# Kernel optimization log

Hardware: AMD Instinct MI355X
Metric: run time of the kernel (lower is better)

## Reference

```python
import jax, jax.numpy as jnp
import numpy as np

B, C, H, W = 8, 512, 96, 96
CK, CV, K = 64, 64, 3  # key/value channels = C/8, kernel_size=3


def setup_inputs() -> dict:
    key = jax.random.key(0)
    ks = jax.random.split(key, 11)
    p = lambda k, shape: jax.random.normal(k, shape, dtype=jnp.float32) * 0.05
    return {
        "x": jax.random.normal(ks[0], (B, C, H, W), dtype=jnp.float32),
        "key1_w": p(ks[1], (CK, C, 1, 1)),
        "key1_b": p(ks[2], (CK,)),
        "key_dw_w": p(ks[3], (CK, 1, K, K)),
        "key_dw_b": p(ks[4], (CK,)),
        "key3_w": p(ks[5], (K * K, CK, 1, 1)),
        "key3_b": p(ks[6], (K * K,)),
        "value_w": p(ks[7], (CV, C, 1, 1)),
        "value_b": p(ks[8], (CV,)),
        "out_w": p(ks[9], (C, CV, 1, 1)),
        "out_b": p(ks[10], (C,)),
    }


def _conv1x1(x, w, b):
    # x: [B,Cin,H,W], w: [Cout,Cin,1,1]
    return jnp.einsum('bchw,oc->bohw', x, w[:, :, 0, 0]) + b[None, :, None, None]


def _unfold3(x):
    # nn.Unfold(kernel_size=3, stride=1, padding=1) then view -> [B,C,9,H,W]
    b, c, h, w = x.shape
    xp = jnp.pad(x, ((0, 0), (0, 0), (1, 1), (1, 1)))
    patches = [xp[:, :, i:i + h, j:j + w] for i in range(3) for j in range(3)]
    return jnp.stack(patches, axis=2)  # [B,C,9,H,W], row-major kernel order like torch


def reference(x, key1_w, key1_b, key_dw_w, key_dw_b, key3_w, key3_b,
              value_w, value_b, out_w, out_b):
    # key branch: 1x1 conv + ReLU -> depthwise 3x3 (no act) -> 1x1 -> k^2 logits
    k = jax.nn.relu(_conv1x1(x, key1_w, key1_b))
    k = jax.lax.conv_general_dilated(
        k, key_dw_w, window_strides=(1, 1), padding='SAME',
        feature_group_count=CK,
        dimension_numbers=('NCHW', 'OIHW', 'NCHW')) + key_dw_b[None, :, None, None]
    k = _conv1x1(k, key3_w, key3_b)            # [B,9,H,W]
    weights = jax.nn.softmax(k[:, None], axis=2)  # [B,1,9,H,W], softmax over kernel taps

    # value branch: 1x1 conv (no act) then unfold 3x3 neighborhoods
    v = _unfold3(_conv1x1(x, value_w, value_b))   # [B,CV,9,H,W]

    y = jnp.sum(weights * v, axis=2)              # [B,CV,H,W]
    return x + _conv1x1(y, out_w, out_b)
```

## Files before the change

### kernel.cpp

```cpp
#include <hip/hip_runtime.h>

#define B_ 8
#define C_ 512
#define H_ 96
#define W_ 96
#define HW_ (H_ * W_)
#define CK_ 64

typedef __attribute__((ext_vector_type(8))) short bf16x8;
typedef __attribute__((ext_vector_type(4))) float f32x4;

#define WPK_OFF ((size_t)192 * HW_)

__device__ __forceinline__ short f2bf(float f) {
    union { float f; unsigned u; } v; v.f = f;
    unsigned r = v.u + 0x7fffu + ((v.u >> 16) & 1u);
    return (short)(r >> 16);
}

__device__ __forceinline__ bf16x8 cvt8(float4 a, float4 b) {
    bf16x8 s;
    s[0] = f2bf(a.x); s[1] = f2bf(a.y); s[2] = f2bf(a.z); s[3] = f2bf(a.w);
    s[4] = f2bf(b.x); s[5] = f2bf(b.y); s[6] = f2bf(b.z); s[7] = f2bf(b.w);
    return s;
}


__global__ void pack_w_kernel(const float* __restrict__ key1_w,
                              const float* __restrict__ value_w,
                              float* __restrict__ outbuf)
{
    const int idx = blockIdx.x * 256 + threadIdx.x;
    const int c8  = idx >> 7;
    const int oc  = idx & 127;
    const float* src = (oc < 64) ? (key1_w + (size_t)oc * C_)
                                 : (value_w + (size_t)(oc - 64) * C_);
    float4 f0 = *(const float4*)(src + c8 * 8);
    float4 f1 = *(const float4*)(src + c8 * 8 + 4);
    short* wpk = (short*)(outbuf + WPK_OFF);
    *(bf16x8*)(wpk + (size_t)idx * 8) = cvt8(f0, f1);
}

__global__ __launch_bounds__(256, 4)
void kv_conv_mfma(const float* __restrict__ x,
                  const float* __restrict__ key1_b,
                  const float* __restrict__ value_b,
                  float* __restrict__ outbuf)
{
    const int b    = blockIdx.y;
    const int px0  = blockIdx.x * 64;
    const int tid  = threadIdx.x;
    const int lane = tid & 63;
    const int w    = tid >> 6;
    const int wm   = w & 1;
    const int wn   = w >> 1;
    const int l15  = lane & 15;
    const int q    = lane >> 4;

    __shared__ float s_bias[128];
    if (tid < 128) s_bias[tid] = (tid < 64) ? key1_b[tid] : value_b[tid - 64];
    __syncthreads();

    f32x4 acc[4][2];
#pragma unroll
    for (int i = 0; i < 4; ++i)
#pragma unroll
        for (int j = 0; j < 2; ++j) acc[i][j] = (f32x4){0.f, 0.f, 0.f, 0.f};

    const short* wpk = (const short*)(outbuf + WPK_OFF);
    const short* apk = wpk + ((size_t)q * 128 + wm * 64 + l15) * 8;
    const float* xq  = x + (size_t)b * C_ * HW_ + (size_t)(q * 8) * HW_
                         + px0 + wn * 32 + l15;

    for (int i = 0; i < 16; ++i) {
        bf16x8 af[4];
#pragma unroll
        for (int mt = 0; mt < 4; ++mt)
            af[mt] = *(const bf16x8*)(apk + ((size_t)i * 512 + mt * 16) * 8);

#pragma unroll
        for (int nt = 0; nt < 2; ++nt) {
            const float* xp = xq + (size_t)i * 32 * HW_ + nt * 16;
            bf16x8 bf;
#pragma unroll
            for (int j = 0; j < 8; ++j) bf[j] = f2bf(xp[(size_t)j * HW_]);
#pragma unroll
            for (int mt = 0; mt < 4; ++mt)
                acc[mt][nt] = __builtin_amdgcn_mfma_f32_16x16x32_bf16(af[mt], bf, acc[mt][nt], 0, 0, 0);
        }
    }

    float* kvb = outbuf + ((size_t)b * C_ + 64) * HW_ + px0;
#pragma unroll
    for (int mt = 0; mt < 4; ++mt) {
#pragma unroll
        for (int r = 0; r < 4; ++r) {
            int oc = wm * 64 + mt * 16 + q * 4 + r;
            float bias = s_bias[oc];
#pragma unroll
            for (int nt = 0; nt < 2; ++nt) {
                float v = acc[mt][nt][r] + bias;
                if (oc < 64) v = fmaxf(v, 0.f);
                kvb[(size_t)oc * HW_ + wn * 32 + nt * 16 + l15] = v;
            }
        }
    }
}

__global__ __launch_bounds__(256, 4)
void attn_kernel(const float* __restrict__ dw_w, const float* __restrict__ dw_b,
                 const float* __restrict__ k3_w, const float* __restrict__ k3_b,
                 float* __restrict__ outbuf)
{
    const int b  = blockIdx.y;
    const int hw = blockIdx.x * 256 + threadIdx.x;
    const int h  = hw / W_;
    const int w  = hw % W_;

    __shared__ float s_dw[CK_ * 9];
    __shared__ float s_dwb[CK_];
    __shared__ float s_k3[9 * CK_];
    __shared__ float s_k3b[16];

    for (int i = threadIdx.x; i < CK_ * 9; i += 256) {
        s_dw[i] = dw_w[i];
        s_k3[i] = k3_w[i];
    }
    if (threadIdx.x < CK_) s_dwb[threadIdx.x] = dw_b[threadIdx.x];
    if (threadIdx.x < 9)   s_k3b[threadIdx.x] = k3_b[threadIdx.x];
    __syncthreads();

    int  off[9];
    bool valid[9];
#pragma unroll
    for (int t = 0; t < 9; ++t) {
        int dy = t / 3 - 1, dx = t % 3 - 1;
        int hh = h + dy, ww = w + dx;
        valid[t] = (hh >= 0) && (hh < H_) && (ww >= 0) && (ww < W_);
        off[t]   = hh * W_ + ww;
    }

    float logits[9];
#pragma unroll
    for (int t = 0; t < 9; ++t) logits[t] = s_k3b[t];

    const float* kb = outbuf + ((size_t)b * C_ + 64) * HW_;
#pragma unroll 4
    for (int c = 0; c < CK_; ++c) {
        const float* kc = kb + (size_t)c * HW_;
        float d = s_dwb[c];
#pragma unroll
        for (int t = 0; t < 9; ++t) {
            float val = valid[t] ? kc[off[t]] : 0.f;
            d = fmaf(s_dw[c * 9 + t], val, d);
        }
#pragma unroll
        for (int t = 0; t < 9; ++t)
            logits[t] = fmaf(s_k3[t * CK_ + c], d, logits[t]);
    }

    float m = logits[0];
#pragma unroll
    for (int t = 1; t < 9; ++t) m = fmaxf(m, logits[t]);
    float e[9], s = 0.f;
#pragma unroll
    for (int t = 0; t < 9; ++t) { e[t] = __expf(logits[t] - m); s += e[t]; }
    float inv = 1.f / s;
    float wt[9];
#pragma unroll
    for (int t = 0; t < 9; ++t) wt[t] = e[t] * inv;

    const float* vb = kb + (size_t)CK_ * HW_;
    float* yb = outbuf + (size_t)b * C_ * HW_;
#pragma unroll 4
    for (int cv = 0; cv < CK_; ++cv) {
        const float* vc = vb + (size_t)cv * HW_;
        float acc = 0.f;
#pragma unroll
        for (int t = 0; t < 9; ++t) {
            float val = valid[t] ? vc[off[t]] : 0.f;
            acc = fmaf(wt[t], val, acc);
        }
        yb[(size_t)cv * HW_ + hw] = acc;
    }
}

__global__ __launch_bounds__(256, 4)
void out_conv_mfma(const float* __restrict__ out_w, const float* __restrict__ out_b,
                   const float* __restrict__ x, float* outbuf, int oc_base)
{
    const int b    = blockIdx.z;
    const int o0   = oc_base + blockIdx.y * 128;
    const int px0  = blockIdx.x * 128;
    const int tid  = threadIdx.x;
    const int lane = tid & 63;
    const int w    = tid >> 6;
    const int wm   = w & 1;
    const int wn   = w >> 1;
    const int l15  = lane & 15;
    const int q    = lane >> 4;

    __shared__ short Ws[128][72];
    __shared__ float s_bias[128];

    {
        int row = tid & 127, half = tid >> 7;
        const float* wp = out_w + (size_t)(o0 + row) * CK_ + half * 32;
        float4 f0 = *(const float4*)(wp);
        float4 f1 = *(const float4*)(wp + 4);
        float4 f2 = *(const float4*)(wp + 8);
        float4 f3 = *(const float4*)(wp + 12);
        float4 f4 = *(const float4*)(wp + 16);
        float4 f5 = *(const float4*)(wp + 20);
        float4 f6 = *(const float4*)(wp + 24);
        float4 f7 = *(const float4*)(wp + 28);
        *(bf16x8*)&Ws[row][half * 32]      = cvt8(f0, f1);
        *(bf16x8*)&Ws[row][half * 32 + 8]  = cvt8(f2, f3);
        *(bf16x8*)&Ws[row][half * 32 + 16] = cvt8(f4, f5);
        *(bf16x8*)&Ws[row][half * 32 + 24] = cvt8(f6, f7);
    }
    if (tid < 128) s_bias[tid] = out_b[o0 + tid];
    __syncthreads();

    f32x4 acc[4][4];
#pragma unroll
    for (int i = 0; i < 4; ++i)
#pragma unroll
        for (int j = 0; j < 4; ++j) acc[i][j] = (f32x4){0.f, 0.f, 0.f, 0.f};

    const float* yb = outbuf + (size_t)b * C_ * HW_ + px0;

#pragma unroll
    for (int kc = 0; kc < CK_; kc += 32) {
        bf16x8 af[4];
#pragma unroll
        for (int mt = 0; mt < 4; ++mt)
            af[mt] = *(bf16x8*)&Ws[wm * 64 + mt * 16 + l15][kc + q * 8];

        const float* yq = yb + (size_t)(kc + q * 8) * HW_ + wn * 64 + l15;
#pragma unroll
        for (int nt = 0; nt < 4; ++nt) {
            const float* yp = yq + nt * 16;
            bf16x8 bf;
#pragma unroll
            for (int j = 0; j < 8; ++j) bf[j] = f2bf(yp[(size_t)j * HW_]);
#pragma unroll
            for (int mt = 0; mt < 4; ++mt)
                acc[mt][nt] = __builtin_amdgcn_mfma_f32_16x16x32_bf16(af[mt], bf, acc[mt][nt], 0, 0, 0);
        }
    }

    __syncthreads();

    const float* xb = x + (size_t)b * C_ * HW_ + px0;
    float* ob       = outbuf + (size_t)b * C_ * HW_ + px0;
#pragma unroll
    for (int mt = 0; mt < 4; ++mt) {
#pragma unroll
        for (int r = 0; r < 4; ++r) {
            int ol   = wm * 64 + mt * 16 + q * 4 + r;
            int oc   = o0 + ol;
            float bias = s_bias[ol];
#pragma unroll
            for (int nt = 0; nt < 4; ++nt) {
                size_t idx = (size_t)oc * HW_ + wn * 64 + nt * 16 + l15;
                ob[idx] = acc[mt][nt][r] + bias + xb[idx];
            }
        }
    }
}

extern "C" void kernel_launch(void* const* d_in, const int* in_sizes, int n_in,
                              void* d_out, int out_size, void* d_ws, size_t ws_size,
                              hipStream_t stream)
{
    const float* x       = (const float*)d_in[0];
    const float* key1_w  = (const float*)d_in[1];
    const float* key1_b  = (const float*)d_in[2];
    const float* dw_w    = (const float*)d_in[3];
    const float* dw_b    = (const float*)d_in[4];
    const float* k3_w    = (const float*)d_in[5];
    const float* k3_b    = (const float*)d_in[6];
    const float* value_w = (const float*)d_in[7];
    const float* value_b = (const float*)d_in[8];
    const float* out_w   = (const float*)d_in[9];
    const float* out_b   = (const float*)d_in[10];
    float* out = (float*)d_out;

    pack_w_kernel<<<dim3(32), dim3(256), 0, stream>>>(key1_w, value_w, out);

    dim3 g1(HW_ / 64, B_);
    kv_conv_mfma<<<g1, dim3(256), 0, stream>>>(x, key1_b, value_b, out);

    dim3 g2(HW_ / 256, B_);
    attn_kernel<<<g2, dim3(256), 0, stream>>>(dw_w, dw_b, k3_w, k3_b, out);

    dim3 g3(HW_ / 128, 3, B_);
    out_conv_mfma<<<g3, dim3(256), 0, stream>>>(out_w, out_b, x, out, 128);

    dim3 g4(HW_ / 128, 1, B_);
    out_conv_mfma<<<g4, dim3(256), 0, stream>>>(out_w, out_b, x, out, 0);
}
```

Baseline: 474.0 us.

## Pre-pack x to bf16 channel-interleaved layout and split attn channels across waves

Adds a pack_x kernel that converts x into bf16 with 8 channels interleaved per pixel, stored in the output buffer. The kv conv can then load B fragments as single 16-byte vector loads instead of eight strided fp32 loads with per-element conversion. The attention kernel now spreads the 64 channels over four waves per 64-pixel tile and reduces the partial logits through shared memory, which gives four times more blocks. The cost is an extra pass over x (read fp32, write bf16) plus an extra launch and a barrier.

```diff
diff --git a/kernel.cpp b/kernel.cpp
--- a/kernel.cpp
+++ b/kernel.cpp
@@ -10,7 +10,8 @@
 typedef __attribute__((ext_vector_type(8))) short bf16x8;
 typedef __attribute__((ext_vector_type(4))) float f32x4;
 
-#define WPK_OFF ((size_t)192 * HW_)
+#define XPK_CH 192
+#define WPK_OFF ((size_t)448 * HW_)
 
 __device__ __forceinline__ short f2bf(float f) {
     union { float f; unsigned u; } v; v.f = f;
@@ -24,7 +25,6 @@
     s[4] = f2bf(b.x); s[5] = f2bf(b.y); s[6] = f2bf(b.z); s[7] = f2bf(b.w);
     return s;
 }
-
 
 __global__ void pack_w_kernel(const float* __restrict__ key1_w,
                               const float* __restrict__ value_w,
@@ -41,9 +41,25 @@
     *(bf16x8*)(wpk + (size_t)idx * 8) = cvt8(f0, f1);
 }
 
+__global__ __launch_bounds__(256)
+void pack_x_kernel(const float* __restrict__ x, float* __restrict__ outbuf)
+{
+    const int px = blockIdx.x * 256 + threadIdx.x;
+    const int c8 = blockIdx.y;
+    const int b  = blockIdx.z;
+    const float* src = x + ((size_t)b * C_ + c8 * 8) * HW_ + px;
+    float f[8];
+#pragma unroll
+    for (int j = 0; j < 8; ++j) f[j] = src[(size_t)j * HW_];
+    bf16x8 s;
+#pragma unroll
+    for (int j = 0; j < 8; ++j) s[j] = f2bf(f[j]);
+    short* xpk = (short*)(outbuf + (size_t)b * C_ * HW_ + (size_t)XPK_CH * HW_);
+    *(bf16x8*)(xpk + ((size_t)c8 * HW_ + px) * 8) = s;
+}
+
 __global__ __launch_bounds__(256, 4)
-void kv_conv_mfma(const float* __restrict__ x,
-                  const float* __restrict__ key1_b,
+void kv_conv_mfma(const float* __restrict__ key1_b,
                   const float* __restrict__ value_b,
                   float* __restrict__ outbuf)
 {
@@ -68,26 +84,24 @@
         for (int j = 0; j < 2; ++j) acc[i][j] = (f32x4){0.f, 0.f, 0.f, 0.f};
 
     const short* wpk = (const short*)(outbuf + WPK_OFF);
+    const short* xpk = (const short*)(outbuf + (size_t)b * C_ * HW_ + (size_t)XPK_CH * HW_);
     const short* apk = wpk + ((size_t)q * 128 + wm * 64 + l15) * 8;
-    const float* xq  = x + (size_t)b * C_ * HW_ + (size_t)(q * 8) * HW_
-                         + px0 + wn * 32 + l15;
+    const short* bpk = xpk + ((size_t)q * HW_ + px0 + wn * 32 + l15) * 8;
 
     for (int i = 0; i < 16; ++i) {
         bf16x8 af[4];
 #pragma unroll
         for (int mt = 0; mt < 4; ++mt)
             af[mt] = *(const bf16x8*)(apk + ((size_t)i * 512 + mt * 16) * 8);
-
-#pragma unroll
-        for (int nt = 0; nt < 2; ++nt) {
-            const float* xp = xq + (size_t)i * 32 * HW_ + nt * 16;
-            bf16x8 bf;
-#pragma unroll
-            for (int j = 0; j < 8; ++j) bf[j] = f2bf(xp[(size_t)j * HW_]);
+        bf16x8 bf[2];
+#pragma unroll
+        for (int nt = 0; nt < 2; ++nt)
+            bf[nt] = *(const bf16x8*)(bpk + ((size_t)(i * 4) * HW_ + nt * 16) * 8);
+#pragma unroll
+        for (int nt = 0; nt < 2; ++nt)
 #pragma unroll
             for (int mt = 0; mt < 4; ++mt)
-                acc[mt][nt] = __builtin_amdgcn_mfma_f32_16x16x32_bf16(af[mt], bf, acc[mt][nt], 0, 0, 0);
-        }
+                acc[mt][nt] = __builtin_amdgcn_mfma_f32_16x16x32_bf16(af[mt], bf[nt], acc[mt][nt], 0, 0, 0);
     }
 
     float* kvb = outbuf + ((size_t)b * C_ + 64) * HW_ + px0;
@@ -112,22 +126,27 @@
                  const float* __restrict__ k3_w, const float* __restrict__ k3_b,
                  float* __restrict__ outbuf)
 {
-    const int b  = blockIdx.y;
-    const int hw = blockIdx.x * 256 + threadIdx.x;
-    const int h  = hw / W_;
-    const int w  = hw % W_;
+    const int b    = blockIdx.y;
+    const int px0  = blockIdx.x * 64;
+    const int tid  = threadIdx.x;
+    const int lane = tid & 63;
+    const int wv   = tid >> 6;
+    const int hw   = px0 + lane;
+    const int h    = hw / W_;
+    const int w    = hw % W_;
 
     __shared__ float s_dw[CK_ * 9];
     __shared__ float s_dwb[CK_];
     __shared__ float s_k3[9 * CK_];
     __shared__ float s_k3b[16];
-
-    for (int i = threadIdx.x; i < CK_ * 9; i += 256) {
+    __shared__ float s_part[4][9][64];
+
+    for (int i = tid; i < CK_ * 9; i += 256) {
         s_dw[i] = dw_w[i];
         s_k3[i] = k3_w[i];
     }
-    if (threadIdx.x < CK_) s_dwb[threadIdx.x] = dw_b[threadIdx.x];
-    if (threadIdx.x < 9)   s_k3b[threadIdx.x] = k3_b[threadIdx.x];
+    if (tid < CK_) s_dwb[tid] = dw_b[tid];
+    if (tid < 9)   s_k3b[tid] = k3_b[tid];
     __syncthreads();
 
     int  off[9];
@@ -140,13 +159,14 @@
         off[t]   = hh * W_ + ww;
     }
 
-    float logits[9];
-#pragma unroll
-    for (int t = 0; t < 9; ++t) logits[t] = s_k3b[t];
+    float part[9];
+#pragma unroll
+    for (int t = 0; t < 9; ++t) part[t] = 0.f;
 
     const float* kb = outbuf + ((size_t)b * C_ + 64) * HW_;
 #pragma unroll 4
-    for (int c = 0; c < CK_; ++c) {
+    for (int ci = 0; ci < 16; ++ci) {
+        const int c = wv * 16 + ci;
         const float* kc = kb + (size_t)c * HW_;
         float d = s_dwb[c];
 #pragma unroll
@@ -156,8 +176,17 @@
         }
 #pragma unroll
         for (int t = 0; t < 9; ++t)
-            logits[t] = fmaf(s_k3[t * CK_ + c], d, logits[t]);
-    }
+            part[t] = fmaf(s_k3[t * CK_ + c], d, part[t]);
+    }
+#pragma unroll
+    for (int t = 0; t < 9; ++t) s_part[wv][t][lane] = part[t];
+    __syncthreads();
+
+    float logits[9];
+#pragma unroll
+    for (int t = 0; t < 9; ++t)
+        logits[t] = s_k3b[t] + s_part[0][t][lane] + s_part[1][t][lane]
+                             + s_part[2][t][lane] + s_part[3][t][lane];
 
     float m = logits[0];
 #pragma unroll
@@ -173,7 +202,8 @@
     const float* vb = kb + (size_t)CK_ * HW_;
     float* yb = outbuf + (size_t)b * C_ * HW_;
 #pragma unroll 4
-    for (int cv = 0; cv < CK_; ++cv) {
+    for (int ci = 0; ci < 16; ++ci) {
+        const int cv = wv * 16 + ci;
         const float* vc = vb + (size_t)cv * HW_;
         float acc = 0.f;
 #pragma unroll
@@ -288,11 +318,12 @@
     float* out = (float*)d_out;
 
     pack_w_kernel<<<dim3(32), dim3(256), 0, stream>>>(key1_w, value_w, out);
+    pack_x_kernel<<<dim3(HW_ / 256, 64, B_), dim3(256), 0, stream>>>(x, out);
 
     dim3 g1(HW_ / 64, B_);
-    kv_conv_mfma<<<g1, dim3(256), 0, stream>>>(x, key1_b, value_b, out);
-
-    dim3 g2(HW_ / 256, B_);
+    kv_conv_mfma<<<g1, dim3(256), 0, stream>>>(key1_b, value_b, out);
+
+    dim3 g2(HW_ / 64, B_);
     attn_kernel<<<g2, dim3(256), 0, stream>>>(dw_w, dw_b, k3_w, k3_b, out);
 
     dim3 g3(HW_ / 128, 3, B_);
```

Measured after the change: 467.6 us. About the same (-1.3%).
